# Kernel tuning notes

Measured on AMD Instinct MI355X. Metric: run time of the kernel, lower is better.

Reference implementation:

```python
import jax, jax.numpy as jnp
import numpy as np

# Stickbreaking attention (IBM ModuleFormer style) as in the torch module:
#   logits = q @ k^T / sqrt(head_dim)  (causal)
#   z = sigmoid(logits), log_beta = logsigmoid(-logits), both causally masked
#   re_cum_log_beta = einsum('bhij,jk->bhik', log_beta, tril(ones(S,S)))
#     -> re[i,k] = sum_{k <= j <= i} log_beta[i, j]   (full tril incl. diagonal,
#        exactly as written in the source: cum_weight = torch.tril(torch.ones(L,L)))
#   weights = z * exp(re_cum_log_beta);  out = weights @ v
# Note: the torch code applies the causal mask by adding -inf; the only finite,
# NaN-free expression of that math (matching ModuleFormer's masked_fill) is to
# zero out masked entries of z and log_beta before the triangular matmul.

B, H, S, D = 2, 16, 1024, 64


def setup_inputs() -> dict:
    key = jax.random.key(0)
    kq, kk, kv = jax.random.split(key, 3)
    q = jax.random.normal(kq, (B, H, S, D), dtype=jnp.float32)
    k = jax.random.normal(kk, (B, H, S, D), dtype=jnp.float32)
    v = jax.random.normal(kv, (B, H, S, D), dtype=jnp.float32)
    return {"q": q, "k": k, "v": v}


def reference(q, k, v):
    head_dim = q.shape[-1]
    scaling = 1.0 / np.sqrt(head_dim).astype(np.float32)
    # [B,H,S,S] attention logits
    logits = jnp.einsum("bhqd,bhkd->bhqk", q, k) * scaling
    seq = logits.shape[-1]
    causal = jnp.tril(jnp.ones((seq, seq), dtype=logits.dtype))  # 1 where j<=i
    z = jax.nn.sigmoid(logits) * causal
    log_beta = jax.nn.log_sigmoid(-logits) * causal
    cum_weight = jnp.tril(jnp.ones((seq, seq), dtype=logits.dtype))
    # re[i,k] = sum_{j>=k} log_beta[i,j] (log_beta already 0 for j>i)
    re_cum_log_beta = jnp.einsum("bhij,jk->bhik", log_beta, cum_weight)
    weights = z * jnp.exp(re_cum_log_beta)
    return jnp.einsum("bhqk,bhkd->bhqd", weights, v)
```

## Files before the change

### kernel.cpp

```cpp
#include <hip/hip_runtime.h>
#include <hip/hip_bf16.h>
#include <math.h>


typedef __attribute__((ext_vector_type(8))) short short8;
typedef __attribute__((ext_vector_type(4))) short short4v;
typedef __attribute__((ext_vector_type(4))) float f32x4;

#define PITCH 72

__device__ inline short bf16r(float x) {
    __hip_bfloat16 h = __float2bfloat16(x);
    return *(short*)&h;
}
__device__ inline float bf16f(short s) {
    union { unsigned u; float f; } c;
    c.u = ((unsigned)(unsigned short)s) << 16;
    return c.f;
}

__global__ __launch_bounds__(256, 2) void stickbreak_mfma(
    const float* __restrict__ Qg, const float* __restrict__ Kg,
    const float* __restrict__ Vg, float* __restrict__ Og)
{
    __shared__ __align__(16) short Kh[64 * PITCH];
    __shared__ __align__(16) short Kl[64 * PITCH];
    __shared__ __align__(16) short Vt[64 * PITCH];
    __shared__ __align__(16) short Ws[64 * PITCH];

    const int t = threadIdx.x;
    const int n = blockIdx.x;
    const int bh = (n & 7) + 8 * (n >> 7);
    const int qr = (n >> 3) & 15;
    const int qt = (n >> 8) ? (15 - qr) : qr;

    const size_t hbase = (size_t)bh * 1024 * 64;
    const float* qp = Qg + hbase + (size_t)qt * 64 * 64;
    const float* kp = Kg + hbase;
    const float* vp = Vg + hbase;
    float*       op = Og + hbase + (size_t)qt * 64 * 64;

    const int lane = t & 63;
    const int wv   = t >> 6;
    const int l16  = lane & 15;
    const int q4   = lane >> 4;

    const int srow = t >> 2;
    const int scol = (t & 3) << 4;
    const int vj   = (t & 15) << 2;
    const int vd   = (t >> 4) << 2;

    short8 qfh[2], qfl[2];
    {
        const float* qrow = qp + (16 * wv + l16) * 64;
        #pragma unroll
        for (int ks = 0; ks < 2; ++ks) {
            const int base = 32 * ks + 8 * q4;
            const float4 f0 = *(const float4*)(qrow + base);
            const float4 f1 = *(const float4*)(qrow + base + 4);
            float a[8] = {f0.x, f0.y, f0.z, f0.w, f1.x, f1.y, f1.z, f1.w};
            #pragma unroll
            for (int j = 0; j < 8; ++j) {
                const short hi = bf16r(a[j]);
                qfh[ks][j] = hi;
                qfl[ks][j] = bf16r(a[j] - bf16f(hi));
            }
        }
    }

    f32x4 Oacc[4];
    #pragma unroll
    for (int i = 0; i < 4; ++i) Oacc[i] = (f32x4){0.f, 0.f, 0.f, 0.f};
    float Crow = 0.f;

    float4 kreg[4], vreg[4];
    {
        const float* ksrc = kp + (size_t)qt * 4096 + srow * 64 + scol;
        const float* vsrc = vp + (size_t)qt * 4096;
        #pragma unroll
        for (int i = 0; i < 4; ++i) kreg[i] = *(const float4*)(ksrc + 4 * i);
        #pragma unroll
        for (int r = 0; r < 4; ++r) vreg[r] = *(const float4*)(vsrc + (vj + r) * 64 + vd);
    }

    for (int kt = qt; kt >= 0; --kt) {
        {
            short8 h0, h1, l0, l1;
            #pragma unroll
            for (int i = 0; i < 4; ++i) {
                float a[4] = {kreg[i].x, kreg[i].y, kreg[i].z, kreg[i].w};
                #pragma unroll
                for (int j = 0; j < 4; ++j) {
                    const short hi = bf16r(a[j]);
                    const short lo = bf16r(a[j] - bf16f(hi));
                    const int idx = 4 * i + j;
                    if (idx < 8) { h0[idx] = hi; l0[idx] = lo; }
                    else         { h1[idx - 8] = hi; l1[idx - 8] = lo; }
                }
            }
            *(short8*)&Kh[srow * PITCH + scol]     = h0;
            *(short8*)&Kh[srow * PITCH + scol + 8] = h1;
            *(short8*)&Kl[srow * PITCH + scol]     = l0;
            *(short8*)&Kl[srow * PITCH + scol + 8] = l1;
        }
        {
            #pragma unroll
            for (int x = 0; x < 4; ++x) {
                float rr[4] = { x == 0 ? vreg[0].x : x == 1 ? vreg[0].y : x == 2 ? vreg[0].z : vreg[0].w,
                                x == 0 ? vreg[1].x : x == 1 ? vreg[1].y : x == 2 ? vreg[1].z : vreg[1].w,
                                x == 0 ? vreg[2].x : x == 1 ? vreg[2].y : x == 2 ? vreg[2].z : vreg[2].w,
                                x == 0 ? vreg[3].x : x == 1 ? vreg[3].y : x == 2 ? vreg[3].z : vreg[3].w };
                short4v w4;
                #pragma unroll
                for (int r = 0; r < 4; ++r) w4[r] = bf16r(rr[r]);
                *(short4v*)&Vt[(vd + x) * PITCH + vj] = w4;
            }
        }
        __syncthreads();

        if (kt > 0) {
            const float* ksrc = kp + (size_t)(kt - 1) * 4096 + srow * 64 + scol;
            const float* vsrc = vp + (size_t)(kt - 1) * 4096;
            #pragma unroll
            for (int i = 0; i < 4; ++i) kreg[i] = *(const float4*)(ksrc + 4 * i);
            #pragma unroll
            for (int r = 0; r < 4; ++r) vreg[r] = *(const float4*)(vsrc + (vj + r) * 64 + vd);
        }

        f32x4 Sacc[4];
        #pragma unroll
        for (int i = 0; i < 4; ++i) Sacc[i] = (f32x4){0.f, 0.f, 0.f, 0.f};
        #pragma unroll
        for (int ks = 0; ks < 2; ++ks) {
            #pragma unroll
            for (int nt = 0; nt < 4; ++nt) {
                const short8 ah = *(const short8*)&Kh[(16 * nt + l16) * PITCH + 32 * ks + 8 * q4];
                const short8 al = *(const short8*)&Kl[(16 * nt + l16) * PITCH + 32 * ks + 8 * q4];
                Sacc[nt] = __builtin_amdgcn_mfma_f32_16x16x32_bf16(ah, qfh[ks], Sacc[nt], 0, 0, 0);
                Sacc[nt] = __builtin_amdgcn_mfma_f32_16x16x32_bf16(al, qfh[ks], Sacc[nt], 0, 0, 0);
                Sacc[nt] = __builtin_amdgcn_mfma_f32_16x16x32_bf16(ah, qfl[ks], Sacc[nt], 0, 0, 0);
            }
        }

        const bool diag = (kt == qt);
        const int irow = 16 * wv + l16;
        float ex[4][4];
        float sR[4];
        #pragma unroll
        for (int nt = 0; nt < 4; ++nt) {
            float lbr[4], lv[4];
            #pragma unroll
            for (int reg = 0; reg < 4; ++reg) {
                float l = Sacc[nt][reg] * 0.125f;
                if (diag && (16 * nt + 4 * q4 + reg > irow)) l = -1e30f;
                const float e  = __expf(-fabsf(l));
                const float lb = -(fmaxf(l, 0.f) + __logf(1.f + e));
                lv[reg] = l; lbr[reg] = lb;
            }
            const float s3 = lbr[3];
            const float s2 = lbr[2] + s3;
            const float s1 = lbr[1] + s2;
            const float s0 = lbr[0] + s1;
            ex[nt][0] = lv[0] + lbr[0] + s0;
            ex[nt][1] = lv[1] + lbr[1] + s1;
            ex[nt][2] = lv[2] + lbr[2] + s2;
            ex[nt][3] = lv[3] + lbr[3] + s3;
            sR[nt] = s0;
        }
        float gq[4], Tn[4];
        #pragma unroll
        for (int nt = 0; nt < 4; ++nt) {
            float g = sR[nt];
            float u = __shfl_down(g, 16, 64); if (q4 < 3) g += u;
            u = __shfl_down(g, 32, 64);       if (q4 < 2) g += u;
            gq[nt] = g;
            Tn[nt] = __shfl(g, l16, 64);
        }
        const float TSa[4] = { Tn[1] + Tn[2] + Tn[3], Tn[2] + Tn[3], Tn[3], 0.f };
        #pragma unroll
        for (int nt = 0; nt < 4; ++nt) {
            const float cross = (gq[nt] - sR[nt]) + TSa[nt] + Crow;
            short4v w4;
            #pragma unroll
            for (int reg = 0; reg < 4; ++reg)
                w4[reg] = bf16r(__expf(ex[nt][reg] + cross));
            *(short4v*)&Ws[irow * PITCH + 16 * nt + 4 * q4] = w4;
        }
        Crow += TSa[0] + Tn[0];

        __syncthreads();

        #pragma unroll
        for (int ks = 0; ks < 2; ++ks) {
            const short8 wa = *(const short8*)&Ws[(16 * wv + l16) * PITCH + 32 * ks + 8 * q4];
            #pragma unroll
            for (int dt = 0; dt < 4; ++dt) {
                const short8 vb = *(const short8*)&Vt[(16 * dt + l16) * PITCH + 32 * ks + 8 * q4];
                Oacc[dt] = __builtin_amdgcn_mfma_f32_16x16x32_bf16(wa, vb, Oacc[dt], 0, 0, 0);
            }
        }

        __syncthreads();
    }

    #pragma unroll
    for (int dt = 0; dt < 4; ++dt)
        #pragma unroll
        for (int r = 0; r < 4; ++r)
            op[(16 * wv + 4 * q4 + r) * 64 + 16 * dt + l16] = Oacc[dt][r];
}

extern "C" void kernel_launch(void* const* d_in, const int* in_sizes, int n_in,
                              void* d_out, int out_size, void* d_ws, size_t ws_size,
                              hipStream_t stream) {
    const float* q = (const float*)d_in[0];
    const float* k = (const float*)d_in[1];
    const float* v = (const float*)d_in[2];
    float* out = (float*)d_out;
    stickbreak_mfma<<<dim3(512), dim3(256), 0, stream>>>(q, k, v, out);
}
```

Before: 105.5 us.

## Precompute bf16 K split and transposed V in prep kernel, double-buffer tiles

A new prep kernel converts each K tile into bf16 hi/lo halves and each V tile into a transposed bf16 tile once. It writes them into the workspace in the padded LDS layout. The main kernel copies these blobs straight into a double-buffered shared tile, so the per-block conversion redone by all 16 query tiles of a head goes away. The block-wide barriers per iteration drop from three to one, since the Ws tile is only read by the wave that wrote it. This costs an extra kernel launch, a workspace round trip, and more shared memory per block, which could limit occupancy.

Result: slower. 128.9 us (+22.2%).

```diff
diff --git a/kernel.cpp b/kernel.cpp
--- a/kernel.cpp
+++ b/kernel.cpp
@@ -8,6 +8,8 @@
 typedef __attribute__((ext_vector_type(4))) float f32x4;
 
 #define PITCH 72
+#define TILE_SH 4608
+#define BLOB_SH 13824
 
 __device__ inline short bf16r(float x) {
     __hip_bfloat16 h = __float2bfloat16(x);
@@ -19,14 +21,64 @@
     return c.f;
 }
 
-__global__ __launch_bounds__(256, 2) void stickbreak_mfma(
-    const float* __restrict__ Qg, const float* __restrict__ Kg,
-    const float* __restrict__ Vg, float* __restrict__ Og)
+__global__ __launch_bounds__(256) void stickbreak_prep(
+    const float* __restrict__ Kg, const float* __restrict__ Vg,
+    short* __restrict__ ws)
 {
-    __shared__ __align__(16) short Kh[64 * PITCH];
-    __shared__ __align__(16) short Kl[64 * PITCH];
-    __shared__ __align__(16) short Vt[64 * PITCH];
-    __shared__ __align__(16) short Ws[64 * PITCH];
+    const int t = threadIdx.x;
+    const int n = blockIdx.x;
+    const float* kp = Kg + (size_t)n * 4096;
+    const float* vp = Vg + (size_t)n * 4096;
+    short* blob = ws + (size_t)n * BLOB_SH;
+
+    {
+        const int srow = t >> 2;
+        const int scol = (t & 3) << 4;
+        const float* src = kp + srow * 64 + scol;
+        short8 h0, h1, l0, l1;
+        #pragma unroll
+        for (int i = 0; i < 16; i += 4) {
+            const float4 f = *(const float4*)(src + i);
+            float a[4] = {f.x, f.y, f.z, f.w};
+            #pragma unroll
+            for (int j = 0; j < 4; ++j) {
+                const short hi = bf16r(a[j]);
+                const short lo = bf16r(a[j] - bf16f(hi));
+                const int idx = i + j;
+                if (idx < 8) { h0[idx] = hi; l0[idx] = lo; }
+                else         { h1[idx - 8] = hi; l1[idx - 8] = lo; }
+            }
+        }
+        *(short8*)&blob[srow * PITCH + scol]               = h0;
+        *(short8*)&blob[srow * PITCH + scol + 8]           = h1;
+        *(short8*)&blob[TILE_SH + srow * PITCH + scol]     = l0;
+        *(short8*)&blob[TILE_SH + srow * PITCH + scol + 8] = l1;
+    }
+    {
+        const int vj = (t & 15) << 2;
+        const int vd = (t >> 4) << 2;
+        float rr[4][4];
+        #pragma unroll
+        for (int r = 0; r < 4; ++r) {
+            const float4 f = *(const float4*)(vp + (vj + r) * 64 + vd);
+            rr[r][0] = f.x; rr[r][1] = f.y; rr[r][2] = f.z; rr[r][3] = f.w;
+        }
+        #pragma unroll
+        for (int x = 0; x < 4; ++x) {
+            short4v w4;
+            #pragma unroll
+            for (int r = 0; r < 4; ++r) w4[r] = bf16r(rr[r][x]);
+            *(short4v*)&blob[2 * TILE_SH + (vd + x) * PITCH + vj] = w4;
+        }
+    }
+}
+
+__global__ __launch_bounds__(256, 2) void stickbreak_main(
+    const float* __restrict__ Qg, const short* __restrict__ ws,
+    float* __restrict__ Og)
+{
+    __shared__ __align__(16) short buf[2][3 * TILE_SH];
+    __shared__ __align__(16) short Ws[TILE_SH];
 
     const int t = threadIdx.x;
     const int n = blockIdx.x;
@@ -36,19 +88,13 @@
 
     const size_t hbase = (size_t)bh * 1024 * 64;
     const float* qp = Qg + hbase + (size_t)qt * 64 * 64;
-    const float* kp = Kg + hbase;
-    const float* vp = Vg + hbase;
+    const short* wsbase = ws + (size_t)bh * 16 * BLOB_SH;
     float*       op = Og + hbase + (size_t)qt * 64 * 64;
 
     const int lane = t & 63;
     const int wv   = t >> 6;
     const int l16  = lane & 15;
     const int q4   = lane >> 4;
-
-    const int srow = t >> 2;
-    const int scol = (t & 3) << 4;
-    const int vj   = (t & 15) << 2;
-    const int vd   = (t >> 4) << 2;
 
     short8 qfh[2], qfl[2];
     {
@@ -73,59 +119,29 @@
     for (int i = 0; i < 4; ++i) Oacc[i] = (f32x4){0.f, 0.f, 0.f, 0.f};
     float Crow = 0.f;
 
-    float4 kreg[4], vreg[4];
-    {
-        const float* ksrc = kp + (size_t)qt * 4096 + srow * 64 + scol;
-        const float* vsrc = vp + (size_t)qt * 4096;
-        #pragma unroll
-        for (int i = 0; i < 4; ++i) kreg[i] = *(const float4*)(ksrc + 4 * i);
-        #pragma unroll
-        for (int r = 0; r < 4; ++r) vreg[r] = *(const float4*)(vsrc + (vj + r) * 64 + vd);
-    }
-
+    {
+        const float4* g = (const float4*)(wsbase + (size_t)qt * BLOB_SH);
+        float4* b = (float4*)buf[0];
+        #pragma unroll
+        for (int c = 0; c < 6; ++c) b[t + 256 * c] = g[t + 256 * c];
+        if (t < 192) b[t + 1536] = g[t + 1536];
+    }
+
+    int p = 0;
+    float4 pf[7];
     for (int kt = qt; kt >= 0; --kt) {
-        {
-            short8 h0, h1, l0, l1;
-            #pragma unroll
-            for (int i = 0; i < 4; ++i) {
-                float a[4] = {kreg[i].x, kreg[i].y, kreg[i].z, kreg[i].w};
-                #pragma unroll
-                for (int j = 0; j < 4; ++j) {
-                    const short hi = bf16r(a[j]);
-                    const short lo = bf16r(a[j] - bf16f(hi));
-                    const int idx = 4 * i + j;
-                    if (idx < 8) { h0[idx] = hi; l0[idx] = lo; }
-                    else         { h1[idx - 8] = hi; l1[idx - 8] = lo; }
-                }
-            }
-            *(short8*)&Kh[srow * PITCH + scol]     = h0;
-            *(short8*)&Kh[srow * PITCH + scol + 8] = h1;
-            *(short8*)&Kl[srow * PITCH + scol]     = l0;
-            *(short8*)&Kl[srow * PITCH + scol + 8] = l1;
-        }
-        {
-            #pragma unroll
-            for (int x = 0; x < 4; ++x) {
-                float rr[4] = { x == 0 ? vreg[0].x : x == 1 ? vreg[0].y : x == 2 ? vreg[0].z : vreg[0].w,
-                                x == 0 ? vreg[1].x : x == 1 ? vreg[1].y : x == 2 ? vreg[1].z : vreg[1].w,
-                                x == 0 ? vreg[2].x : x == 1 ? vreg[2].y : x == 2 ? vreg[2].z : vreg[2].w,
-                                x == 0 ? vreg[3].x : x == 1 ? vreg[3].y : x == 2 ? vreg[3].z : vreg[3].w };
-                short4v w4;
-                #pragma unroll
-                for (int r = 0; r < 4; ++r) w4[r] = bf16r(rr[r]);
-                *(short4v*)&Vt[(vd + x) * PITCH + vj] = w4;
-            }
-        }
         __syncthreads();
 
         if (kt > 0) {
-            const float* ksrc = kp + (size_t)(kt - 1) * 4096 + srow * 64 + scol;
-            const float* vsrc = vp + (size_t)(kt - 1) * 4096;
-            #pragma unroll
-            for (int i = 0; i < 4; ++i) kreg[i] = *(const float4*)(ksrc + 4 * i);
-            #pragma unroll
-            for (int r = 0; r < 4; ++r) vreg[r] = *(const float4*)(vsrc + (vj + r) * 64 + vd);
-        }
+            const float4* g = (const float4*)(wsbase + (size_t)(kt - 1) * BLOB_SH);
+            #pragma unroll
+            for (int c = 0; c < 6; ++c) pf[c] = g[t + 256 * c];
+            if (t < 192) pf[6] = g[t + 1536];
+        }
+
+        const short* Kh = &buf[p][0];
+        const short* Kl = &buf[p][TILE_SH];
+        const short* Vt = &buf[p][2 * TILE_SH];
 
         f32x4 Sacc[4];
         #pragma unroll
@@ -188,7 +204,12 @@
         }
         Crow += TSa[0] + Tn[0];
 
-        __syncthreads();
+        if (kt > 0) {
+            float4* b = (float4*)buf[p ^ 1];
+            #pragma unroll
+            for (int c = 0; c < 6; ++c) b[t + 256 * c] = pf[c];
+            if (t < 192) b[t + 1536] = pf[6];
+        }
 
         #pragma unroll
         for (int ks = 0; ks < 2; ++ks) {
@@ -200,7 +221,7 @@
             }
         }
 
-        __syncthreads();
+        p ^= 1;
     }
 
     #pragma unroll
@@ -217,5 +238,7 @@
     const float* k = (const float*)d_in[1];
     const float* v = (const float*)d_in[2];
     float* out = (float*)d_out;
-    stickbreak_mfma<<<dim3(512), dim3(256), 0, stream>>>(q, k, v, out);
-}
+    short* ws = (short*)d_ws;
+    stickbreak_prep<<<dim3(512), dim3(256), 0, stream>>>(k, v, ws);
+    stickbreak_main<<<dim3(512), dim3(256), 0, stream>>>(q, ws, out);
+}
```
